# Kernel optimization log

Hardware: AMD Instinct MI355X
Metric: run time of the kernel (lower is better)

## Reference

```python
import jax, jax.numpy as jnp
import numpy as np

N, E, DIN, DOUT = 50000, 625000, 128, 128


def setup_inputs() -> dict:
    key = jax.random.key(0)
    k = jax.random.split(key, 4)
    x = jax.random.normal(k[0], (N, DIN), dtype=jnp.float32)
    edge_index = jax.random.randint(k[1], (2, E), 0, N, dtype=jnp.int32)
    s = 1.0 / np.sqrt(DIN)  # Glorot-ish init like torch Linear
    W_fwd = jax.random.uniform(k[2], (DIN, DOUT), jnp.float32, -s, s)
    W_bwd = jax.random.uniform(k[3], (DIN, DOUT), jnp.float32, -s, s)
    b_fwd = jnp.zeros((DOUT,), jnp.float32)
    b_bwd = jnp.zeros((DOUT,), jnp.float32)
    return {"x": x, "edge_index": edge_index, "W_fwd": W_fwd, "b_fwd": b_fwd,
            "W_bwd": W_bwd, "b_bwd": b_bwd}


def gcn_conv(x, W, b, src, dst, n):
    """PyG GCNConv: add self-loops, symmetric degree norm, gather-scatter aggregate."""
    loops = jnp.arange(n, dtype=src.dtype)
    src2 = jnp.concatenate([src, loops])  # [E+N]
    dst2 = jnp.concatenate([dst, loops])
    ones = jnp.ones(src2.shape[0], dtype=x.dtype)
    deg = jax.ops.segment_sum(ones, dst2, num_segments=n)  # in-degree incl. self-loop
    dinv = jnp.where(deg > 0, jax.lax.rsqrt(deg), 0.0)
    norm = dinv[src2] * dinv[dst2]  # [E+N]
    h = x @ W  # [N, DOUT] dense GEMM before message passing
    msgs = h[src2] * norm[:, None]  # gather + scale, [E+N, DOUT]
    out = jax.ops.segment_sum(msgs, dst2, num_segments=n)  # scatter-add
    return out + b


def reference(x, edge_index, W_fwd, b_fwd, W_bwd, b_bwd):
    src, dst = edge_index[0], edge_index[1]
    n = x.shape[0]
    x_forward = gcn_conv(x, W_fwd, b_fwd, src, dst, n)
    # reversed edge direction for the backward diffusion conv
    x_backward = gcn_conv(x, W_bwd, b_bwd, dst, src, n)
    # dropout omitted (eval mode / deterministic reference)
    return jax.nn.relu(x_forward + x_backward)
```

## Files before the change

### kernel.cpp

```cpp
#include <hip/hip_runtime.h>
#include <hip/hip_bf16.h>
#include <cstdint>

static constexpr int BLK      = 256;
static constexpr int CAP      = 40;
static constexpr int BINSHIFT = 8;
static constexpr int BINNODES = 1 << BINSHIFT;
static constexpr int BINCAP   = BINNODES * CAP / 2;
static constexpr int EPB      = 2048;
static constexpr int OVMAX    = 1024;
static constexpr int NB2MAX   = 512;

typedef __attribute__((ext_vector_type(8))) short bf16x8;
typedef __attribute__((ext_vector_type(4))) float f32x4;

__device__ __forceinline__ float bf16lo(uint32_t u) { return __uint_as_float(u << 16); }
__device__ __forceinline__ float bf16hi(uint32_t u) { return __uint_as_float(u & 0xffff0000u); }
__device__ __forceinline__ unsigned short f2bf(float f) {
    __hip_bfloat16 h = __float2bfloat16(f);
    return *(unsigned short*)&h;
}

__global__ __launch_bounds__(BLK) void k_bin(
        const int* __restrict__ src, const int* __restrict__ dst, int ne,
        uint32_t* __restrict__ pair, int* __restrict__ gcnt,
        int* __restrict__ ovcnt, int* __restrict__ ovlist, int nbins) {
    __shared__ uint32_t stage[EPB * 2];
    __shared__ int hist[NB2MAX];
    __shared__ int lofs[NB2MAX];
    __shared__ int gbase[NB2MAX];
    __shared__ int chunk[NB2MAX / 8];
    const int tid = threadIdx.x, bid = blockIdx.x;
    const int nb2 = 2 * nbins;
    for (int i = tid; i < nb2; i += BLK) hist[i] = 0;
    __syncthreads();

    int s[8], d[8];
    const int e0 = bid * EPB + tid;
#pragma unroll
    for (int k = 0; k < 8; ++k) {
        int e = e0 + k * BLK;
        bool v = e < ne;
        s[k] = v ? src[e] : -1;
        d[k] = v ? dst[e] : -1;
        if (v) {
            atomicAdd(&hist[d[k] >> BINSHIFT], 1);
            atomicAdd(&hist[nbins + (s[k] >> BINSHIFT)], 1);
        }
    }
    __syncthreads();

    const int nch = (nb2 + 7) >> 3;
    if (tid < nch) {
        int a = 0, base = tid << 3;
#pragma unroll
        for (int k = 0; k < 8; ++k) { int idx = base + k; if (idx < nb2) a += hist[idx]; }
        chunk[tid] = a;
    }
    __syncthreads();
    if (tid == 0) { int a = 0; for (int c = 0; c < nch; ++c) { int t = chunk[c]; chunk[c] = a; a += t; } }
    __syncthreads();
    for (int i = tid; i < nb2; i += BLK) {
        int a = chunk[i >> 3];
        for (int k = (i >> 3) << 3; k < i; ++k) a += hist[k];
        lofs[i] = a;
    }
    __syncthreads();
    for (int i = tid; i < nb2; i += BLK) {
        int c = hist[i];
        gbase[i] = c ? atomicAdd(&gcnt[i], c) : 0;
        hist[i] = lofs[i];
    }
    __syncthreads();
#pragma unroll
    for (int k = 0; k < 8; ++k) {
        if (s[k] >= 0) {
            int b0 = d[k] >> BINSHIFT;
            int p0 = atomicAdd(&hist[b0], 1);
            stage[p0] = ((uint32_t)d[k] << 16) | (uint32_t)s[k];
            int b1 = nbins + (s[k] >> BINSHIFT);
            int p1 = atomicAdd(&hist[b1], 1);
            stage[p1] = ((uint32_t)s[k] << 16) | (uint32_t)d[k];
        }
    }
    __syncthreads();
    int nval = ne - bid * EPB; if (nval > EPB) nval = EPB; if (nval < 0) nval = 0;
    const int total = 2 * nval;
    for (int i = tid; i < total; i += BLK) {
        int lo = 0, hi = nb2 - 1;
        while (lo < hi) { int mid = (lo + hi + 1) >> 1; if (lofs[mid] <= i) lo = mid; else hi = mid - 1; }
        int gidx = gbase[lo] + (i - lofs[lo]);
        if (gidx < BINCAP)
            pair[(size_t)lo * BINCAP + gidx] = stage[i];
        else {
            int node = (int)(stage[i] >> 16);
            int q = atomicAdd(ovcnt, 1);
            if (q < OVMAX) ovlist[q] = (node << 1) | (lo >= nbins ? 1 : 0);
        }
    }
}

__global__ __launch_bounds__(BLK) void k_build_conv(
        uint32_t* __restrict__ pair, const int* __restrict__ gcnt,
        int* __restrict__ cnt_f, int* __restrict__ cnt_b,
        float* __restrict__ dinv_f, float* __restrict__ dinv_b,
        int* __restrict__ ovcnt, int* __restrict__ ovlist,
        const float* __restrict__ x, uint32_t* __restrict__ xb32, int nxw, int gxc,
        const float* __restrict__ Wf, const float* __restrict__ Wb,
        unsigned short* __restrict__ WTf, unsigned short* __restrict__ WTb,
        int n, int nbins) {
    const int bid = blockIdx.x, tid = threadIdx.x;
    const int nb2 = 2 * nbins;
    if (bid < nb2) {
        __shared__ unsigned short buck[BINNODES * CAP];
        __shared__ int lcnt[BINNODES];
        lcnt[tid] = 0;
        __syncthreads();
        int count = gcnt[bid]; if (count > BINCAP) count = BINCAP;
        const uint32_t* pb = pair + (size_t)bid * BINCAP;
        const int dir = bid >= nbins ? 1 : 0;
        for (int i = tid; i < count; i += BLK) {
            uint32_t p = pb[i];
            int l = (p >> 16) & (BINNODES - 1);
            int r = atomicAdd(&lcnt[l], 1);
            if (r < CAP) buck[l * CAP + r] = (unsigned short)(p & 0xffffu);
            else {
                int q = atomicAdd(ovcnt, 1);
                if (q < OVMAX)
                    ovlist[q] = (((((bid - dir * nbins) << BINSHIFT) + l)) << 1) | dir;
            }
        }
        __syncthreads();
        const int node = ((bid - dir * nbins) << BINSHIFT) + tid;
        if (node < n) {
            int c = lcnt[tid];
            if (dir) { cnt_b[node] = c; dinv_b[node] = rsqrtf(1.0f + (float)c); }
            else     { cnt_f[node] = c; dinv_f[node] = rsqrtf(1.0f + (float)c); }
        }
        uint32_t* seg = pair + (size_t)bid * BINCAP;
        const uint32_t* b32 = (const uint32_t*)buck;
        for (int i = tid; i < BINCAP; i += BLK) seg[i] = b32[i];
        return;
    }
    if (bid < nb2 + gxc) {
        int base = (bid - nb2) * 2048;
        int end = base + 2048; if (end > nxw) end = nxw;
        for (int i = base + tid; i < end; i += BLK) {
            float2 v = ((const float2*)x)[i];
            xb32[i] = ((uint32_t)f2bf(v.y) << 16) | (uint32_t)f2bf(v.x);
        }
        return;
    }
    int wb = bid - nb2 - gxc;
    for (int idx = wb * 2048 + tid; idx < (wb + 1) * 2048; idx += BLK) {
        int c = idx >> 7, k = idx & 127;
        WTf[c * 128 + k] = f2bf(Wf[k * 128 + c]);
        WTb[c * 128 + k] = f2bf(Wb[k * 128 + c]);
    }
}

__device__ __forceinline__ void accum_range(
        int j0, int j1, int ofs, float sc,
        const uint32_t* __restrict__ xb, int lane, float& a0, float& a1) {
    int j = j0;
    for (; j + 8 <= j1; j += 8) {
        int   o0 = __shfl(ofs, j + 0), o1 = __shfl(ofs, j + 1);
        int   o2 = __shfl(ofs, j + 2), o3 = __shfl(ofs, j + 3);
        int   o4 = __shfl(ofs, j + 4), o5 = __shfl(ofs, j + 5);
        int   o6 = __shfl(ofs, j + 6), o7 = __shfl(ofs, j + 7);
        float s0 = __shfl(sc, j + 0), s1 = __shfl(sc, j + 1);
        float s2 = __shfl(sc, j + 2), s3 = __shfl(sc, j + 3);
        float s4 = __shfl(sc, j + 4), s5 = __shfl(sc, j + 5);
        float s6 = __shfl(sc, j + 6), s7 = __shfl(sc, j + 7);
        uint32_t u0 = xb[(size_t)(o0 + lane)], u1 = xb[(size_t)(o1 + lane)];
        uint32_t u2 = xb[(size_t)(o2 + lane)], u3 = xb[(size_t)(o3 + lane)];
        uint32_t u4 = xb[(size_t)(o4 + lane)], u5 = xb[(size_t)(o5 + lane)];
        uint32_t u6 = xb[(size_t)(o6 + lane)], u7 = xb[(size_t)(o7 + lane)];
        a0 = fmaf(s0, bf16lo(u0), a0); a1 = fmaf(s0, bf16hi(u0), a1);
        a0 = fmaf(s1, bf16lo(u1), a0); a1 = fmaf(s1, bf16hi(u1), a1);
        a0 = fmaf(s2, bf16lo(u2), a0); a1 = fmaf(s2, bf16hi(u2), a1);
        a0 = fmaf(s3, bf16lo(u3), a0); a1 = fmaf(s3, bf16hi(u3), a1);
        a0 = fmaf(s4, bf16lo(u4), a0); a1 = fmaf(s4, bf16hi(u4), a1);
        a0 = fmaf(s5, bf16lo(u5), a0); a1 = fmaf(s5, bf16hi(u5), a1);
        a0 = fmaf(s6, bf16lo(u6), a0); a1 = fmaf(s6, bf16hi(u6), a1);
        a0 = fmaf(s7, bf16lo(u7), a0); a1 = fmaf(s7, bf16hi(u7), a1);
    }
    for (; j + 4 <= j1; j += 4) {
        int   o0 = __shfl(ofs, j + 0), o1 = __shfl(ofs, j + 1);
        int   o2 = __shfl(ofs, j + 2), o3 = __shfl(ofs, j + 3);
        float s0 = __shfl(sc, j + 0), s1 = __shfl(sc, j + 1);
        float s2 = __shfl(sc, j + 2), s3 = __shfl(sc, j + 3);
        uint32_t u0 = xb[(size_t)(o0 + lane)], u1 = xb[(size_t)(o1 + lane)];
        uint32_t u2 = xb[(size_t)(o2 + lane)], u3 = xb[(size_t)(o3 + lane)];
        a0 = fmaf(s0, bf16lo(u0), a0); a1 = fmaf(s0, bf16hi(u0), a1);
        a0 = fmaf(s1, bf16lo(u1), a0); a1 = fmaf(s1, bf16hi(u1), a1);
        a0 = fmaf(s2, bf16lo(u2), a0); a1 = fmaf(s2, bf16hi(u2), a1);
        a0 = fmaf(s3, bf16lo(u3), a0); a1 = fmaf(s3, bf16hi(u3), a1);
    }
    for (; j < j1; ++j) {
        int oj = __shfl(ofs, j); float sj = __shfl(sc, j);
        uint32_t uj = xb[(size_t)(oj + lane)];
        a0 = fmaf(sj, bf16lo(uj), a0); a1 = fmaf(sj, bf16hi(uj), a1);
    }
}

__global__ __launch_bounds__(BLK) void k_gather_agg(
        const int* __restrict__ cnt_f, const int* __restrict__ cnt_b,
        const unsigned short* __restrict__ adj_f,
        const unsigned short* __restrict__ adj_b,
        const float* __restrict__ dinv_f, const float* __restrict__ dinv_b,
        const uint32_t* __restrict__ xb32,
        uint32_t* __restrict__ agg32,
        int n, int gnode,
        const int* __restrict__ ovcnt, const int* __restrict__ ovlist,
        const int* __restrict__ src, const int* __restrict__ dst, int ne) {
    const int bid = blockIdx.x;
    if (bid < gnode) {
        const int wave = threadIdx.x >> 6;
        const int lane = threadIdx.x & 63;
        const int node = bid * 4 + wave;
        if (node >= n) return;

        int cf = cnt_f[node], cb = cnt_b[node];
        if (cf > CAP || cb > CAP) return;

        float dvsf = dinv_f[node], dvsb = dinv_b[node];
        uint32_t uv = xb32[(size_t)node * 64 + lane];
        float accf0 = dvsf * dvsf * bf16lo(uv), accf1 = dvsf * dvsf * bf16hi(uv);
        float accb0 = dvsb * dvsb * bf16lo(uv), accb1 = dvsb * dvsb * bf16hi(uv);

        const int mt = cf + cb;
        if (mt <= 64) {
            int ofs = 0; float sc = 0.f;
            if (lane < cf) {
                int nb = adj_f[node * CAP + lane];
                ofs = nb * 64;
                sc  = dvsf * dinv_f[nb];
            } else if (lane < mt) {
                int nb = adj_b[node * CAP + (lane - cf)];
                ofs = nb * 64;
                sc  = dvsb * dinv_b[nb];
            }
            accum_range(0,  cf, ofs, sc, xb32, lane, accf0, accf1);
            accum_range(cf, mt, ofs, sc, xb32, lane, accb0, accb1);
        } else {
            for (int j = 0; j < cf; ++j) {
                int nb = adj_f[node * CAP + j];
                float dj = dvsf * dinv_f[nb];
                uint32_t u = xb32[(size_t)nb * 64 + lane];
                accf0 = fmaf(dj, bf16lo(u), accf0); accf1 = fmaf(dj, bf16hi(u), accf1);
            }
            for (int j = 0; j < cb; ++j) {
                int nb = adj_b[node * CAP + j];
                float dj = dvsb * dinv_b[nb];
                uint32_t u = xb32[(size_t)nb * 64 + lane];
                accb0 = fmaf(dj, bf16lo(u), accb0); accb1 = fmaf(dj, bf16hi(u), accb1);
            }
        }
        agg32[(size_t)node * 128 + lane] =
            ((uint32_t)f2bf(accf1) << 16) | (uint32_t)f2bf(accf0);
        agg32[(size_t)node * 128 + 64 + lane] =
            ((uint32_t)f2bf(accb1) << 16) | (uint32_t)f2bf(accb0);
        return;
    }

    int nov = *ovcnt; if (nov > OVMAX) nov = OVMAX;
    if (nov == 0) return;
    __shared__ int lst[4096];
    __shared__ int lc;
    const int tid = threadIdx.x;
    for (int i = bid - gnode; i < nov; i += 8) {
        int node = ovlist[i] >> 1;
        for (int d2 = 0; d2 < 2; ++d2) {
            const int* key = d2 ? src : dst;
            const int* val = d2 ? dst : src;
            const float* dinv = d2 ? dinv_b : dinv_f;
            float dvs = dinv[node];
            float s0 = 0.f, s1 = 0.f;
            if (tid < 64) {
                uint32_t u = xb32[(size_t)node * 64 + tid];
                s0 = dvs * bf16lo(u); s1 = dvs * bf16hi(u);
            }
            for (int start = 0; start < ne; start += 4096) {
                if (tid == 0) lc = 0;
                __syncthreads();
                int end = min(start + 4096, ne);
                for (int e2 = start + tid; e2 < end; e2 += BLK)
                    if (key[e2] == node) { int q = atomicAdd(&lc, 1); lst[q] = val[e2]; }
                __syncthreads();
                int mm = lc;
                if (tid < 64) {
                    for (int j = 0; j < mm; ++j) {
                        int nb = lst[j];
                        float dv = dinv[nb];
                        uint32_t u = xb32[(size_t)nb * 64 + tid];
                        s0 = fmaf(dv, bf16lo(u), s0);
                        s1 = fmaf(dv, bf16hi(u), s1);
                    }
                }
                __syncthreads();
            }
            if (tid < 64) {
                float a0 = dvs * s0, a1 = dvs * s1;
                agg32[(size_t)node * 128 + d2 * 64 + tid] =
                    ((uint32_t)f2bf(a1) << 16) | (uint32_t)f2bf(a0);
            }
            __syncthreads();
        }
    }
}

__global__ __launch_bounds__(BLK) void k_gemm_out(
        const unsigned short* __restrict__ agg,
        const unsigned short* __restrict__ WTf,
        const unsigned short* __restrict__ WTb,
        const float* __restrict__ bfv, const float* __restrict__ bbv,
        float* __restrict__ out, int n) {
    const int wave = threadIdx.x >> 6, lane = threadIdx.x & 63;
    const int wm = wave >> 1, wh = wave & 1;
    const int q = lane >> 4, t16 = lane & 15;
    const int m0 = blockIdx.x * 32 + wm * 16;
    int arow = m0 + t16; if (arow >= n) arow = n - 1;
    const unsigned short* ra = agg + (size_t)arow * 256;
    bf16x8 af[4], ab[4];
#pragma unroll
    for (int s = 0; s < 4; ++s) {
        af[s] = *(const bf16x8*)(ra + s * 32 + q * 8);
        ab[s] = *(const bf16x8*)(ra + 128 + s * 32 + q * 8);
    }
    __syncthreads();
#pragma unroll
    for (int t = 0; t < 4; ++t) {
        const int col = wh * 64 + t * 16 + t16;
        const unsigned short* wrf = WTf + (size_t)col * 128;
        const unsigned short* wrb = WTb + (size_t)col * 128;
        f32x4 c = {0.f, 0.f, 0.f, 0.f};
#pragma unroll
        for (int s = 0; s < 4; ++s)
            c = __builtin_amdgcn_mfma_f32_16x16x32_bf16(
                    af[s], *(const bf16x8*)(wrf + s * 32 + q * 8), c, 0, 0, 0);
#pragma unroll
        for (int s = 0; s < 4; ++s)
            c = __builtin_amdgcn_mfma_f32_16x16x32_bf16(
                    ab[s], *(const bf16x8*)(wrb + s * 32 + q * 8), c, 0, 0, 0);
        const float bias = bfv[col] + bbv[col];
#pragma unroll
        for (int r = 0; r < 4; ++r) {
            int row = m0 + q * 4 + r;
            if (row < n)
                out[(size_t)row * 128 + col] = fmaxf(c[r] + bias, 0.f);
        }
    }
}

extern "C" void kernel_launch(void* const* d_in, const int* in_sizes, int n_in,
                              void* d_out, int out_size, void* d_ws, size_t ws_size,
                              hipStream_t stream) {
    const float* x  = (const float*)d_in[0];
    const int*   ei = (const int*)d_in[1];
    const float* Wf = (const float*)d_in[2];
    const float* bf = (const float*)d_in[3];
    const float* Wb = (const float*)d_in[4];
    const float* bb = (const float*)d_in[5];

    const int n  = in_sizes[0] / 128;
    const int ne = in_sizes[1] / 2;
    const int* src = ei;
    const int* dst = ei + ne;
    float* out = (float*)d_out;

    const int nbins = (n + BINNODES - 1) >> BINSHIFT;
    const int nb2   = 2 * nbins;

    char* w = (char*)d_ws;
    uint32_t* pair = (uint32_t*)w;              w += (size_t)nb2 * BINCAP * 4;
    uint32_t* xb32 = (uint32_t*)w;              w += (size_t)n * 64 * 4;
    float* dinv_f = (float*)w;                  w += (size_t)n * 4;
    float* dinv_b = (float*)w;                  w += (size_t)n * 4;
    unsigned short* WTf = (unsigned short*)w;   w += 128 * 128 * 2;
    unsigned short* WTb = (unsigned short*)w;   w += 128 * 128 * 2;
    int* cnt_f = (int*)w;                       w += (size_t)n * 4;
    int* cnt_b = (int*)w;                       w += (size_t)n * 4;
    int* gcnt = (int*)w;                        w += (size_t)nb2 * 4;
    int* ovcnt = (int*)w;                       w += 8 * 4;
    int* ovlist = (int*)w;                      w += OVMAX * 4;

    const unsigned short* adj_f = (const unsigned short*)pair;
    const unsigned short* adj_b = adj_f + (size_t)nbins * BINNODES * CAP;
    uint32_t* agg32 = (uint32_t*)d_out;

    const int gbin  = (ne + EPB - 1) / EPB;
    const int gxc   = (n * 64 + 2047) / 2048;
    const int gnode = (n + 3) / 4;
    const int ggo   = (n + 31) / 32;

    hipMemsetAsync(gcnt, 0, (size_t)(nb2 + 8) * 4, stream);

    k_bin<<<gbin, BLK, 0, stream>>>(src, dst, ne, pair, gcnt, ovcnt, ovlist, nbins);

    k_build_conv<<<nb2 + gxc + 8, BLK, 0, stream>>>(pair, gcnt,
                                                    cnt_f, cnt_b, dinv_f, dinv_b,
                                                    ovcnt, ovlist,
                                                    x, xb32, n * 64, gxc,
                                                    Wf, Wb, WTf, WTb, n, nbins);

    k_gather_agg<<<gnode + 8, BLK, 0, stream>>>(cnt_f, cnt_b, adj_f, adj_b,
                                                dinv_f, dinv_b, xb32,
                                                agg32, n, gnode,
                                                ovcnt, ovlist, src, dst, ne);

    k_gemm_out<<<ggo, BLK, 0, stream>>>((const unsigned short*)agg32,
                                        WTf, WTb, bf, bb, out, n);
}
```

Before: 199.4 us.

## Fuse gather-aggregate with output GEMM and move conversions into binning kernel

Merges the gather/aggregation kernel with the MFMA output GEMM, so each block aggregates 16 nodes into shared memory and multiplies them directly, with no bf16 aggregate round trip through global memory. The x/W bf16 conversion blocks move into the binning kernel, which now stores each staged entry's bin index so the per-element binary search is gone. Edges per binning block are halved for more parallelism, and overflow nodes get a scalar fallback GEMM in the tail blocks. This cuts one launch and one global intermediate, but gather blocks are larger and hold a barrier before the MFMA stage.

```diff
diff --git a/kernel.cpp b/kernel.cpp
--- a/kernel.cpp
+++ b/kernel.cpp
@@ -7,7 +7,7 @@
 static constexpr int BINSHIFT = 8;
 static constexpr int BINNODES = 1 << BINSHIFT;
 static constexpr int BINCAP   = BINNODES * CAP / 2;
-static constexpr int EPB      = 2048;
+static constexpr int EPB      = 1024;
 static constexpr int OVMAX    = 1024;
 static constexpr int NB2MAX   = 512;
 
@@ -16,147 +16,149 @@
 
 __device__ __forceinline__ float bf16lo(uint32_t u) { return __uint_as_float(u << 16); }
 __device__ __forceinline__ float bf16hi(uint32_t u) { return __uint_as_float(u & 0xffff0000u); }
+__device__ __forceinline__ float bf16f(unsigned short u) { return __uint_as_float((uint32_t)u << 16); }
 __device__ __forceinline__ unsigned short f2bf(float f) {
     __hip_bfloat16 h = __float2bfloat16(f);
     return *(unsigned short*)&h;
 }
 
-__global__ __launch_bounds__(BLK) void k_bin(
+__global__ __launch_bounds__(BLK) void k_bin_conv(
         const int* __restrict__ src, const int* __restrict__ dst, int ne,
         uint32_t* __restrict__ pair, int* __restrict__ gcnt,
-        int* __restrict__ ovcnt, int* __restrict__ ovlist, int nbins) {
-    __shared__ uint32_t stage[EPB * 2];
-    __shared__ int hist[NB2MAX];
-    __shared__ int lofs[NB2MAX];
-    __shared__ int gbase[NB2MAX];
-    __shared__ int chunk[NB2MAX / 8];
-    const int tid = threadIdx.x, bid = blockIdx.x;
-    const int nb2 = 2 * nbins;
-    for (int i = tid; i < nb2; i += BLK) hist[i] = 0;
-    __syncthreads();
-
-    int s[8], d[8];
-    const int e0 = bid * EPB + tid;
-#pragma unroll
-    for (int k = 0; k < 8; ++k) {
-        int e = e0 + k * BLK;
-        bool v = e < ne;
-        s[k] = v ? src[e] : -1;
-        d[k] = v ? dst[e] : -1;
-        if (v) {
-            atomicAdd(&hist[d[k] >> BINSHIFT], 1);
-            atomicAdd(&hist[nbins + (s[k] >> BINSHIFT)], 1);
-        }
-    }
-    __syncthreads();
-
-    const int nch = (nb2 + 7) >> 3;
-    if (tid < nch) {
-        int a = 0, base = tid << 3;
-#pragma unroll
-        for (int k = 0; k < 8; ++k) { int idx = base + k; if (idx < nb2) a += hist[idx]; }
-        chunk[tid] = a;
-    }
-    __syncthreads();
-    if (tid == 0) { int a = 0; for (int c = 0; c < nch; ++c) { int t = chunk[c]; chunk[c] = a; a += t; } }
-    __syncthreads();
-    for (int i = tid; i < nb2; i += BLK) {
-        int a = chunk[i >> 3];
-        for (int k = (i >> 3) << 3; k < i; ++k) a += hist[k];
-        lofs[i] = a;
-    }
-    __syncthreads();
-    for (int i = tid; i < nb2; i += BLK) {
-        int c = hist[i];
-        gbase[i] = c ? atomicAdd(&gcnt[i], c) : 0;
-        hist[i] = lofs[i];
-    }
-    __syncthreads();
-#pragma unroll
-    for (int k = 0; k < 8; ++k) {
-        if (s[k] >= 0) {
-            int b0 = d[k] >> BINSHIFT;
-            int p0 = atomicAdd(&hist[b0], 1);
-            stage[p0] = ((uint32_t)d[k] << 16) | (uint32_t)s[k];
-            int b1 = nbins + (s[k] >> BINSHIFT);
-            int p1 = atomicAdd(&hist[b1], 1);
-            stage[p1] = ((uint32_t)s[k] << 16) | (uint32_t)d[k];
-        }
-    }
-    __syncthreads();
-    int nval = ne - bid * EPB; if (nval > EPB) nval = EPB; if (nval < 0) nval = 0;
-    const int total = 2 * nval;
-    for (int i = tid; i < total; i += BLK) {
-        int lo = 0, hi = nb2 - 1;
-        while (lo < hi) { int mid = (lo + hi + 1) >> 1; if (lofs[mid] <= i) lo = mid; else hi = mid - 1; }
-        int gidx = gbase[lo] + (i - lofs[lo]);
-        if (gidx < BINCAP)
-            pair[(size_t)lo * BINCAP + gidx] = stage[i];
-        else {
-            int node = (int)(stage[i] >> 16);
-            int q = atomicAdd(ovcnt, 1);
-            if (q < OVMAX) ovlist[q] = (node << 1) | (lo >= nbins ? 1 : 0);
-        }
-    }
-}
-
-__global__ __launch_bounds__(BLK) void k_build_conv(
+        int* __restrict__ ovcnt, int* __restrict__ ovlist, int nbins, int gbin,
+        const float* __restrict__ x, uint32_t* __restrict__ xb32, int nxw, int gxc,
+        const float* __restrict__ Wf, const float* __restrict__ Wb,
+        unsigned short* __restrict__ WTf, unsigned short* __restrict__ WTb) {
+    const int bid = blockIdx.x, tid = threadIdx.x;
+    if (bid < gbin) {
+        __shared__ uint32_t stage[EPB * 2];
+        __shared__ unsigned short binof[EPB * 2];
+        __shared__ int hist[NB2MAX];
+        __shared__ int lofs[NB2MAX];
+        __shared__ int gbase[NB2MAX];
+        __shared__ int chunk[NB2MAX / 8];
+        const int nb2 = 2 * nbins;
+        for (int i = tid; i < nb2; i += BLK) hist[i] = 0;
+        __syncthreads();
+
+        int s[4], d[4];
+        const int e0 = bid * EPB + tid;
+#pragma unroll
+        for (int k = 0; k < 4; ++k) {
+            int e = e0 + k * BLK;
+            bool v = e < ne;
+            s[k] = v ? src[e] : -1;
+            d[k] = v ? dst[e] : -1;
+            if (v) {
+                atomicAdd(&hist[d[k] >> BINSHIFT], 1);
+                atomicAdd(&hist[nbins + (s[k] >> BINSHIFT)], 1);
+            }
+        }
+        __syncthreads();
+
+        const int nch = (nb2 + 7) >> 3;
+        if (tid < nch) {
+            int a = 0, base = tid << 3;
+#pragma unroll
+            for (int k = 0; k < 8; ++k) { int idx = base + k; if (idx < nb2) a += hist[idx]; }
+            chunk[tid] = a;
+        }
+        __syncthreads();
+        if (tid == 0) { int a = 0; for (int c = 0; c < nch; ++c) { int t = chunk[c]; chunk[c] = a; a += t; } }
+        __syncthreads();
+        for (int i = tid; i < nb2; i += BLK) {
+            int a = chunk[i >> 3];
+            for (int k = (i >> 3) << 3; k < i; ++k) a += hist[k];
+            lofs[i] = a;
+        }
+        __syncthreads();
+        for (int i = tid; i < nb2; i += BLK) {
+            int c = hist[i];
+            gbase[i] = c ? atomicAdd(&gcnt[i], c) : 0;
+            hist[i] = lofs[i];
+        }
+        __syncthreads();
+#pragma unroll
+        for (int k = 0; k < 4; ++k) {
+            if (s[k] >= 0) {
+                int b0 = d[k] >> BINSHIFT;
+                int p0 = atomicAdd(&hist[b0], 1);
+                stage[p0] = ((uint32_t)d[k] << 16) | (uint32_t)s[k];
+                binof[p0] = (unsigned short)b0;
+                int b1 = nbins + (s[k] >> BINSHIFT);
+                int p1 = atomicAdd(&hist[b1], 1);
+                stage[p1] = ((uint32_t)s[k] << 16) | (uint32_t)d[k];
+                binof[p1] = (unsigned short)b1;
+            }
+        }
+        __syncthreads();
+        int nval = ne - bid * EPB; if (nval > EPB) nval = EPB; if (nval < 0) nval = 0;
+        const int total = 2 * nval;
+        for (int i = tid; i < total; i += BLK) {
+            int b = binof[i];
+            int gidx = gbase[b] + (i - lofs[b]);
+            if (gidx < BINCAP)
+                pair[(size_t)b * BINCAP + gidx] = stage[i];
+            else {
+                int node = (int)(stage[i] >> 16);
+                int q = atomicAdd(ovcnt, 1);
+                if (q < OVMAX) ovlist[q] = (node << 1) | (b >= nbins ? 1 : 0);
+            }
+        }
+        return;
+    }
+    if (bid < gbin + gxc) {
+        int base = (bid - gbin) * 2048;
+        int end = base + 2048; if (end > nxw) end = nxw;
+        for (int i = base + tid; i < end; i += BLK) {
+            float2 v = ((const float2*)x)[i];
+            xb32[i] = ((uint32_t)f2bf(v.y) << 16) | (uint32_t)f2bf(v.x);
+        }
+        return;
+    }
+    int wb = bid - gbin - gxc;
+    for (int idx = wb * 2048 + tid; idx < (wb + 1) * 2048; idx += BLK) {
+        int c = idx >> 7, k = idx & 127;
+        WTf[c * 128 + k] = f2bf(Wf[k * 128 + c]);
+        WTb[c * 128 + k] = f2bf(Wb[k * 128 + c]);
+    }
+}
+
+__global__ __launch_bounds__(BLK) void k_build(
         uint32_t* __restrict__ pair, const int* __restrict__ gcnt,
         int* __restrict__ cnt_f, int* __restrict__ cnt_b,
         float* __restrict__ dinv_f, float* __restrict__ dinv_b,
         int* __restrict__ ovcnt, int* __restrict__ ovlist,
-        const float* __restrict__ x, uint32_t* __restrict__ xb32, int nxw, int gxc,
-        const float* __restrict__ Wf, const float* __restrict__ Wb,
-        unsigned short* __restrict__ WTf, unsigned short* __restrict__ WTb,
         int n, int nbins) {
     const int bid = blockIdx.x, tid = threadIdx.x;
-    const int nb2 = 2 * nbins;
-    if (bid < nb2) {
-        __shared__ unsigned short buck[BINNODES * CAP];
-        __shared__ int lcnt[BINNODES];
-        lcnt[tid] = 0;
-        __syncthreads();
-        int count = gcnt[bid]; if (count > BINCAP) count = BINCAP;
-        const uint32_t* pb = pair + (size_t)bid * BINCAP;
-        const int dir = bid >= nbins ? 1 : 0;
-        for (int i = tid; i < count; i += BLK) {
-            uint32_t p = pb[i];
-            int l = (p >> 16) & (BINNODES - 1);
-            int r = atomicAdd(&lcnt[l], 1);
-            if (r < CAP) buck[l * CAP + r] = (unsigned short)(p & 0xffffu);
-            else {
-                int q = atomicAdd(ovcnt, 1);
-                if (q < OVMAX)
-                    ovlist[q] = (((((bid - dir * nbins) << BINSHIFT) + l)) << 1) | dir;
-            }
-        }
-        __syncthreads();
-        const int node = ((bid - dir * nbins) << BINSHIFT) + tid;
-        if (node < n) {
-            int c = lcnt[tid];
-            if (dir) { cnt_b[node] = c; dinv_b[node] = rsqrtf(1.0f + (float)c); }
-            else     { cnt_f[node] = c; dinv_f[node] = rsqrtf(1.0f + (float)c); }
-        }
-        uint32_t* seg = pair + (size_t)bid * BINCAP;
-        const uint32_t* b32 = (const uint32_t*)buck;
-        for (int i = tid; i < BINCAP; i += BLK) seg[i] = b32[i];
-        return;
-    }
-    if (bid < nb2 + gxc) {
-        int base = (bid - nb2) * 2048;
-        int end = base + 2048; if (end > nxw) end = nxw;
-        for (int i = base + tid; i < end; i += BLK) {
-            float2 v = ((const float2*)x)[i];
-            xb32[i] = ((uint32_t)f2bf(v.y) << 16) | (uint32_t)f2bf(v.x);
-        }
-        return;
-    }
-    int wb = bid - nb2 - gxc;
-    for (int idx = wb * 2048 + tid; idx < (wb + 1) * 2048; idx += BLK) {
-        int c = idx >> 7, k = idx & 127;
-        WTf[c * 128 + k] = f2bf(Wf[k * 128 + c]);
-        WTb[c * 128 + k] = f2bf(Wb[k * 128 + c]);
-    }
+    __shared__ unsigned short buck[BINNODES * CAP];
+    __shared__ int lcnt[BINNODES];
+    lcnt[tid] = 0;
+    __syncthreads();
+    int count = gcnt[bid]; if (count > BINCAP) count = BINCAP;
+    const uint32_t* pb = pair + (size_t)bid * BINCAP;
+    const int dir = bid >= nbins ? 1 : 0;
+    for (int i = tid; i < count; i += BLK) {
+        uint32_t p = pb[i];
+        int l = (p >> 16) & (BINNODES - 1);
+        int r = atomicAdd(&lcnt[l], 1);
+        if (r < CAP) buck[l * CAP + r] = (unsigned short)(p & 0xffffu);
+        else {
+            int q = atomicAdd(ovcnt, 1);
+            if (q < OVMAX)
+                ovlist[q] = (((((bid - dir * nbins) << BINSHIFT) + l)) << 1) | dir;
+        }
+    }
+    __syncthreads();
+    const int node = ((bid - dir * nbins) << BINSHIFT) + tid;
+    if (node < n) {
+        int c = lcnt[tid];
+        if (dir) { cnt_b[node] = c; dinv_b[node] = rsqrtf(1.0f + (float)c); }
+        else     { cnt_f[node] = c; dinv_f[node] = rsqrtf(1.0f + (float)c); }
+    }
+    uint32_t* seg = pair + (size_t)bid * BINCAP;
+    const uint32_t* b32 = (const uint32_t*)buck;
+    for (int i = tid; i < BINCAP; i += BLK) seg[i] = b32[i];
 }
 
 __device__ __forceinline__ void accum_range(
@@ -204,72 +206,110 @@
     }
 }
 
-__global__ __launch_bounds__(BLK) void k_gather_agg(
+__global__ __launch_bounds__(BLK) void k_gather_gemm(
         const int* __restrict__ cnt_f, const int* __restrict__ cnt_b,
         const unsigned short* __restrict__ adj_f,
         const unsigned short* __restrict__ adj_b,
         const float* __restrict__ dinv_f, const float* __restrict__ dinv_b,
         const uint32_t* __restrict__ xb32,
-        uint32_t* __restrict__ agg32,
-        int n, int gnode,
+        const unsigned short* __restrict__ WTf,
+        const unsigned short* __restrict__ WTb,
+        const float* __restrict__ bfv, const float* __restrict__ bbv,
+        float* __restrict__ out, int n, int gnode2,
         const int* __restrict__ ovcnt, const int* __restrict__ ovlist,
         const int* __restrict__ src, const int* __restrict__ dst, int ne) {
-    const int bid = blockIdx.x;
-    if (bid < gnode) {
-        const int wave = threadIdx.x >> 6;
-        const int lane = threadIdx.x & 63;
-        const int node = bid * 4 + wave;
-        if (node >= n) return;
-
-        int cf = cnt_f[node], cb = cnt_b[node];
-        if (cf > CAP || cb > CAP) return;
-
-        float dvsf = dinv_f[node], dvsb = dinv_b[node];
-        uint32_t uv = xb32[(size_t)node * 64 + lane];
-        float accf0 = dvsf * dvsf * bf16lo(uv), accf1 = dvsf * dvsf * bf16hi(uv);
-        float accb0 = dvsb * dvsb * bf16lo(uv), accb1 = dvsb * dvsb * bf16hi(uv);
-
-        const int mt = cf + cb;
-        if (mt <= 64) {
-            int ofs = 0; float sc = 0.f;
-            if (lane < cf) {
-                int nb = adj_f[node * CAP + lane];
-                ofs = nb * 64;
-                sc  = dvsf * dinv_f[nb];
-            } else if (lane < mt) {
-                int nb = adj_b[node * CAP + (lane - cf)];
-                ofs = nb * 64;
-                sc  = dvsb * dinv_b[nb];
-            }
-            accum_range(0,  cf, ofs, sc, xb32, lane, accf0, accf1);
-            accum_range(cf, mt, ofs, sc, xb32, lane, accb0, accb1);
-        } else {
-            for (int j = 0; j < cf; ++j) {
-                int nb = adj_f[node * CAP + j];
-                float dj = dvsf * dinv_f[nb];
-                uint32_t u = xb32[(size_t)nb * 64 + lane];
-                accf0 = fmaf(dj, bf16lo(u), accf0); accf1 = fmaf(dj, bf16hi(u), accf1);
-            }
-            for (int j = 0; j < cb; ++j) {
-                int nb = adj_b[node * CAP + j];
-                float dj = dvsb * dinv_b[nb];
-                uint32_t u = xb32[(size_t)nb * 64 + lane];
-                accb0 = fmaf(dj, bf16lo(u), accb0); accb1 = fmaf(dj, bf16hi(u), accb1);
-            }
-        }
-        agg32[(size_t)node * 128 + lane] =
-            ((uint32_t)f2bf(accf1) << 16) | (uint32_t)f2bf(accf0);
-        agg32[(size_t)node * 128 + 64 + lane] =
-            ((uint32_t)f2bf(accb1) << 16) | (uint32_t)f2bf(accb0);
+    __shared__ uint32_t aggL[16 * 132];
+    __shared__ int ovflag[16];
+    __shared__ int lst[2048];
+    __shared__ int lc;
+    const int bid = blockIdx.x, tid = threadIdx.x;
+    if (bid < gnode2) {
+        const int wave = tid >> 6, lane = tid & 63;
+        const int node0 = bid * 16;
+        for (int i4 = 0; i4 < 4; ++i4) {
+            const int row = wave * 4 + i4;
+            const int node = node0 + row;
+            int cf = 0, cb = 0;
+            bool skip = node >= n;
+            if (!skip) { cf = cnt_f[node]; cb = cnt_b[node]; skip = (cf > CAP || cb > CAP); }
+            if (lane == 0) ovflag[row] = skip ? 1 : 0;
+            if (skip) continue;
+
+            float dvsf = dinv_f[node], dvsb = dinv_b[node];
+            uint32_t uv = xb32[(size_t)node * 64 + lane];
+            float accf0 = dvsf * dvsf * bf16lo(uv), accf1 = dvsf * dvsf * bf16hi(uv);
+            float accb0 = dvsb * dvsb * bf16lo(uv), accb1 = dvsb * dvsb * bf16hi(uv);
+
+            const int mt = cf + cb;
+            if (mt <= 64) {
+                int ofs = 0; float sc = 0.f;
+                if (lane < cf) {
+                    int nb = adj_f[node * CAP + lane];
+                    ofs = nb * 64;
+                    sc  = dvsf * dinv_f[nb];
+                } else if (lane < mt) {
+                    int nb = adj_b[node * CAP + (lane - cf)];
+                    ofs = nb * 64;
+                    sc  = dvsb * dinv_b[nb];
+                }
+                accum_range(0,  cf, ofs, sc, xb32, lane, accf0, accf1);
+                accum_range(cf, mt, ofs, sc, xb32, lane, accb0, accb1);
+            } else {
+                for (int j = 0; j < cf; ++j) {
+                    int nb = adj_f[node * CAP + j];
+                    float dj = dvsf * dinv_f[nb];
+                    uint32_t u = xb32[(size_t)nb * 64 + lane];
+                    accf0 = fmaf(dj, bf16lo(u), accf0); accf1 = fmaf(dj, bf16hi(u), accf1);
+                }
+                for (int j = 0; j < cb; ++j) {
+                    int nb = adj_b[node * CAP + j];
+                    float dj = dvsb * dinv_b[nb];
+                    uint32_t u = xb32[(size_t)nb * 64 + lane];
+                    accb0 = fmaf(dj, bf16lo(u), accb0); accb1 = fmaf(dj, bf16hi(u), accb1);
+                }
+            }
+            aggL[row * 132 + lane] =
+                ((uint32_t)f2bf(accf1) << 16) | (uint32_t)f2bf(accf0);
+            aggL[row * 132 + 64 + lane] =
+                ((uint32_t)f2bf(accb1) << 16) | (uint32_t)f2bf(accb0);
+        }
+        __syncthreads();
+
+        const int q = lane >> 4, t16 = lane & 15;
+        bf16x8 a[8];
+#pragma unroll
+        for (int s = 0; s < 8; ++s)
+            a[s] = *(const bf16x8*)((const char*)aggL + t16 * 528 + s * 64 + q * 16);
+#pragma unroll
+        for (int t2 = 0; t2 < 2; ++t2) {
+            const int col = (wave * 2 + t2) * 16 + t16;
+            const unsigned short* wrf = WTf + (size_t)col * 128;
+            const unsigned short* wrb = WTb + (size_t)col * 128;
+            f32x4 c = {0.f, 0.f, 0.f, 0.f};
+#pragma unroll
+            for (int s = 0; s < 4; ++s)
+                c = __builtin_amdgcn_mfma_f32_16x16x32_bf16(
+                        a[s], *(const bf16x8*)(wrf + s * 32 + q * 8), c, 0, 0, 0);
+#pragma unroll
+            for (int s = 0; s < 4; ++s)
+                c = __builtin_amdgcn_mfma_f32_16x16x32_bf16(
+                        a[4 + s], *(const bf16x8*)(wrb + s * 32 + q * 8), c, 0, 0, 0);
+            const float bias = bfv[col] + bbv[col];
+#pragma unroll
+            for (int r = 0; r < 4; ++r) {
+                int row = q * 4 + r;
+                int node = node0 + row;
+                if (node < n && !ovflag[row])
+                    out[(size_t)node * 128 + col] = fmaxf(c[r] + bias, 0.f);
+            }
+        }
         return;
     }
 
     int nov = *ovcnt; if (nov > OVMAX) nov = OVMAX;
     if (nov == 0) return;
-    __shared__ int lst[4096];
-    __shared__ int lc;
-    const int tid = threadIdx.x;
-    for (int i = bid - gnode; i < nov; i += 8) {
+    float* aggfl = (float*)aggL;
+    for (int i = bid - gnode2; i < nov; i += 8) {
         int node = ovlist[i] >> 1;
         for (int d2 = 0; d2 < 2; ++d2) {
             const int* key = d2 ? src : dst;
@@ -281,12 +321,12 @@
                 uint32_t u = xb32[(size_t)node * 64 + tid];
                 s0 = dvs * bf16lo(u); s1 = dvs * bf16hi(u);
             }
-            for (int start = 0; start < ne; start += 4096) {
+            for (int start = 0; start < ne; start += 2048) {
                 if (tid == 0) lc = 0;
                 __syncthreads();
-                int end = min(start + 4096, ne);
+                int end = min(start + 2048, ne);
                 for (int e2 = start + tid; e2 < end; e2 += BLK)
-                    if (key[e2] == node) { int q = atomicAdd(&lc, 1); lst[q] = val[e2]; }
+                    if (key[e2] == node) { int qq = atomicAdd(&lc, 1); lst[qq] = val[e2]; }
                 __syncthreads();
                 int mm = lc;
                 if (tid < 64) {
@@ -301,55 +341,23 @@
                 __syncthreads();
             }
             if (tid < 64) {
-                float a0 = dvs * s0, a1 = dvs * s1;
-                agg32[(size_t)node * 128 + d2 * 64 + tid] =
-                    ((uint32_t)f2bf(a1) << 16) | (uint32_t)f2bf(a0);
+                aggfl[d2 * 128 + 2 * tid]     = bf16f(f2bf(dvs * s0));
+                aggfl[d2 * 128 + 2 * tid + 1] = bf16f(f2bf(dvs * s1));
             }
             __syncthreads();
         }
-    }
-}
-
-__global__ __launch_bounds__(BLK) void k_gemm_out(
-        const unsigned short* __restrict__ agg,
-        const unsigned short* __restrict__ WTf,
-        const unsigned short* __restrict__ WTb,
-        const float* __restrict__ bfv, const float* __restrict__ bbv,
-        float* __restrict__ out, int n) {
-    const int wave = threadIdx.x >> 6, lane = threadIdx.x & 63;
-    const int wm = wave >> 1, wh = wave & 1;
-    const int q = lane >> 4, t16 = lane & 15;
-    const int m0 = blockIdx.x * 32 + wm * 16;
-    int arow = m0 + t16; if (arow >= n) arow = n - 1;
-    const unsigned short* ra = agg + (size_t)arow * 256;
-    bf16x8 af[4], ab[4];
-#pragma unroll
-    for (int s = 0; s < 4; ++s) {
-        af[s] = *(const bf16x8*)(ra + s * 32 + q * 8);
-        ab[s] = *(const bf16x8*)(ra + 128 + s * 32 + q * 8);
-    }
-    __syncthreads();
-#pragma unroll
-    for (int t = 0; t < 4; ++t) {
-        const int col = wh * 64 + t * 16 + t16;
-        const unsigned short* wrf = WTf + (size_t)col * 128;
-        const unsigned short* wrb = WTb + (size_t)col * 128;
-        f32x4 c = {0.f, 0.f, 0.f, 0.f};
-#pragma unroll
-        for (int s = 0; s < 4; ++s)
-            c = __builtin_amdgcn_mfma_f32_16x16x32_bf16(
-                    af[s], *(const bf16x8*)(wrf + s * 32 + q * 8), c, 0, 0, 0);
-#pragma unroll
-        for (int s = 0; s < 4; ++s)
-            c = __builtin_amdgcn_mfma_f32_16x16x32_bf16(
-                    ab[s], *(const bf16x8*)(wrb + s * 32 + q * 8), c, 0, 0, 0);
-        const float bias = bfv[col] + bbv[col];
-#pragma unroll
-        for (int r = 0; r < 4; ++r) {
-            int row = m0 + q * 4 + r;
-            if (row < n)
-                out[(size_t)row * 128 + col] = fmaxf(c[r] + bias, 0.f);
-        }
+        if (tid < 128) {
+            const int col = tid;
+            float acc = bfv[col] + bbv[col];
+            const unsigned short* wrf = WTf + (size_t)col * 128;
+            const unsigned short* wrb = WTb + (size_t)col * 128;
+            for (int k = 0; k < 128; ++k) {
+                acc = fmaf(aggfl[k],       bf16f(wrf[k]), acc);
+                acc = fmaf(aggfl[128 + k], bf16f(wrb[k]), acc);
+            }
+            out[(size_t)node * 128 + col] = fmaxf(acc, 0.f);
+        }
+        __syncthreads();
     }
 }
 
@@ -387,28 +395,25 @@
 
     const unsigned short* adj_f = (const unsigned short*)pair;
     const unsigned short* adj_b = adj_f + (size_t)nbins * BINNODES * CAP;
-    uint32_t* agg32 = (uint32_t*)d_out;
-
-    const int gbin  = (ne + EPB - 1) / EPB;
-    const int gxc   = (n * 64 + 2047) / 2048;
-    const int gnode = (n + 3) / 4;
-    const int ggo   = (n + 31) / 32;
+
+    const int gbin   = (ne + EPB - 1) / EPB;
+    const int gxc    = (n * 64 + 2047) / 2048;
+    const int gnode2 = (n + 15) / 16;
 
     hipMemsetAsync(gcnt, 0, (size_t)(nb2 + 8) * 4, stream);
 
-    k_bin<<<gbin, BLK, 0, stream>>>(src, dst, ne, pair, gcnt, ovcnt, ovlist, nbins);
-
-    k_build_conv<<<nb2 + gxc + 8, BLK, 0, stream>>>(pair, gcnt,
-                                                    cnt_f, cnt_b, dinv_f, dinv_b,
-                                                    ovcnt, ovlist,
-                                                    x, xb32, n * 64, gxc,
-                                                    Wf, Wb, WTf, WTb, n, nbins);
-
-    k_gather_agg<<<gnode + 8, BLK, 0, stream>>>(cnt_f, cnt_b, adj_f, adj_b,
-                                                dinv_f, dinv_b, xb32,
-                                                agg32, n, gnode,
-                                                ovcnt, ovlist, src, dst, ne);
-
-    k_gemm_out<<<ggo, BLK, 0, stream>>>((const unsigned short*)agg32,
-                                        WTf, WTb, bf, bb, out, n);
-}
+    k_bin_conv<<<gbin + gxc + 8, BLK, 0, stream>>>(src, dst, ne,
+                                                   pair, gcnt, ovcnt, ovlist,
+                                                   nbins, gbin,
+                                                   x, xb32, n * 64, gxc,
+                                                   Wf, Wb, WTf, WTb);
+
+    k_build<<<nb2, BLK, 0, stream>>>(pair, gcnt, cnt_f, cnt_b,
+                                     dinv_f, dinv_b, ovcnt, ovlist, n, nbins);
+
+    k_gather_gemm<<<gnode2 + 8, BLK, 0, stream>>>(cnt_f, cnt_b, adj_f, adj_b,
+                                                  dinv_f, dinv_b, xb32,
+                                                  WTf, WTb, bf, bb,
+                                                  out, n, gnode2,
+                                                  ovcnt, ovlist, src, dst, ne);
+}
```

Result: faster. 181.0 us (-9.2%).
